# Kernel tuning notes

Hardware: AMD Instinct MI355X
Metric: run time of the kernel (lower is better)

Reference implementation:

```python
import jax, jax.numpy as jnp
import numpy as np

EMB_DIM = 512
HIDDEN = 512
NODE_DIM = 256
NUM_NODES = 64
L_RNN = 3
BATCH = 2048


def setup_inputs() -> dict:
    key = jax.random.key(0)
    ks = jax.random.split(key, 8)
    s = 0.05

    def rn(k, shape):
        return jax.random.normal(k, shape, dtype=jnp.float32) * s

    return {
        "emb": jax.random.normal(ks[0], (BATCH, EMB_DIM), dtype=jnp.float32),
        "Win1": rn(ks[1], (HIDDEN, EMB_DIM)),
        "bin1": jnp.zeros((HIDDEN,), jnp.float32),
        "Win2": rn(ks[2], (L_RNN * HIDDEN, HIDDEN)),
        "bin2": jnp.zeros((L_RNN * HIDDEN,), jnp.float32),
        "Wih": rn(ks[3], (L_RNN, 4 * HIDDEN, HIDDEN)),
        "Whh": rn(ks[4], (L_RNN, 4 * HIDDEN, HIDDEN)),
        "bih": jnp.zeros((L_RNN, 4 * HIDDEN), jnp.float32),
        "bhh": jnp.zeros((L_RNN, 4 * HIDDEN), jnp.float32),
        "Wout1": rn(ks[5], (HIDDEN, HIDDEN)),
        "bout1": jnp.zeros((HIDDEN,), jnp.float32),
        "Wout2": rn(ks[6], (NODE_DIM, HIDDEN)),
        "bout2": jnp.zeros((NODE_DIM,), jnp.float32),
    }


def reference(emb, Win1, bin1, Win2, bin2, Wih, Whh, bih, bhh,
              Wout1, bout1, Wout2, bout2):
    B = emb.shape[0]
    # FNN_in: emb -> initial hidden states for all LSTM layers
    hx = jax.nn.relu(emb @ Win1.T + bin1) @ Win2.T + bin2      # [B, L*H]
    hx = hx.reshape(B, L_RNN, HIDDEN).transpose(1, 0, 2)        # [L, B, H]
    cx = jnp.zeros_like(hx)
    x0 = jnp.zeros((B, HIDDEN), dtype=emb.dtype)                # first input (zeros)

    def step(carry, _):
        h, c, x = carry
        hs, cs = [], []
        inp = x
        for l in range(L_RNN):  # small fixed layer loop
            g = inp @ Wih[l].T + bih[l] + h[l] @ Whh[l].T + bhh[l]  # [B, 4H]
            i, f, gg, o = jnp.split(g, 4, axis=-1)  # PyTorch gate order i,f,g,o
            c_new = jax.nn.sigmoid(f) * c[l] + jax.nn.sigmoid(i) * jnp.tanh(gg)
            h_new = jax.nn.sigmoid(o) * jnp.tanh(c_new)
            hs.append(h_new)
            cs.append(c_new)
            inp = h_new
        return (jnp.stack(hs), jnp.stack(cs), inp), inp

    _, ys = jax.lax.scan(step, (hx, cx, x0), None, length=NUM_NODES)  # [T, B, H]

    x = ys.transpose(1, 0, 2).reshape(B * NUM_NODES, HIDDEN)    # [B*T, H]
    x = jax.nn.relu(x @ Wout1.T + bout1) @ Wout2.T + bout2      # FNN_out
    return x.reshape(B, NUM_NODES, NODE_DIM)
```

## Files before the change

### kernel.cpp

```cpp
#include <hip/hip_runtime.h>
#include <hip/hip_bf16.h>
#include <cstdint>
#include <cstddef>

using bf16 = __hip_bfloat16;
typedef short bf16x8 __attribute__((ext_vector_type(8)));
typedef float f32x4 __attribute__((ext_vector_type(4)));

#define CHUNK 16

__device__ __forceinline__ float fsigmoid(float x) {
  return 1.0f / (1.0f + __expf(-x));
}
__device__ __forceinline__ float ftanh_(float x) {
  float e = __expf(-2.0f * fabsf(x));
  float t = (1.0f - e) / (1.0f + e);
  return copysignf(t, x);
}

__device__ __forceinline__ void gload_lds16(const void* g, void* l) {
  __builtin_amdgcn_global_load_lds(
      (const __attribute__((address_space(1))) void*)g,
      (__attribute__((address_space(3))) void*)l, 16, 0, 0);
}

__global__ void cvt_bf16_kernel(const float* __restrict__ in, bf16* __restrict__ out, int n) {
  int i = blockIdx.x * blockDim.x + threadIdx.x;
  int stride = gridDim.x * blockDim.x;
  for (; i < n; i += stride) out[i] = __float2bfloat16(in[i]);
}

__global__ void build_wf_kernel(const float* __restrict__ Wih, const float* __restrict__ Whh,
                                const float* __restrict__ bih, const float* __restrict__ bhh,
                                bf16* __restrict__ Wf, float* __restrict__ bfused) {
  int i = blockIdx.x * 256 + threadIdx.x;
  int k = i & 1023;
  int r = (i >> 10) & 2047;
  int l = i >> 21;
  int u = r >> 6, gate = (r >> 4) & 3, v = r & 15;
  int j = u * 16 + v;
  int srow = l * 2048 + gate * 512 + j;
  float val = (k < 512) ? Wih[(size_t)srow * 512 + k] : Whh[(size_t)srow * 512 + (k - 512)];
  Wf[i] = __float2bfloat16(val);
  if (k == 0) bfused[l * 2048 + r] = bih[srow] + bhh[srow];
}

template <int EPI>
__global__ __launch_bounds__(512) void gemm_bt(
    const bf16* __restrict__ A0, const bf16* __restrict__ A1,
    const bf16* __restrict__ Bw, const float* __restrict__ bias,
    void* __restrict__ out0, void* __restrict__ out1, void* __restrict__ out2,
    float* __restrict__ cst,
    int K, int lda, int ldo, int aux) {
  const int tid = threadIdx.x;
  const int wave = tid >> 6;
  const int lane = tid & 63;

  const int gx = gridDim.x;
  const int nwg = gx * gridDim.y;
  const int flat = blockIdx.x + gx * blockIdx.y;
  int m0, n0;
  if (gx == 16 && gridDim.y == 16) {
    const int xcd = flat & 7;
    const int w = flat >> 3;
    const int mt = (xcd >> 2) * 8 + (w & 7);
    const int nt = (xcd & 3) * 4 + (w >> 3);
    m0 = mt * 128;
    n0 = nt * 128;
  } else {
    const int v = (flat & 7) * (nwg >> 3) + (flat >> 3);
    m0 = (v % gx) * 128;
    n0 = (v / gx) * 128;
  }

  const int wr = wave >> 1, wc = wave & 1;

  __shared__ alignas(16) short ls[4 * 16384];
  char* lsb = (char*)ls;

  f32x4 acc[2][4];
#pragma unroll
  for (int i = 0; i < 2; ++i)
#pragma unroll
    for (int j = 0; j < 4; ++j) acc[i][j] = (f32x4){0.f, 0.f, 0.f, 0.f};

  const int s_row = tid >> 3;
  const int s_k = (((tid & 7) ^ ((tid >> 3) & 7)) * 8);
  const int l16 = lane & 15;
  const int khi = lane >> 4;
  const int sx = l16 & 7;

  const int nk = K >> 6;

  auto stage = [&](int step) {
    int b = step & 3;
    int kt = step << 6;
    const bf16* as = A0;
    int kk = kt;
    if (kt >= 512) { as = A1; kk = kt - 512; }
    char* base = lsb + b * 32768;
    gload_lds16(as + (size_t)(m0 + s_row) * lda + kk + s_k, base + tid * 16);
    gload_lds16(as + (size_t)(m0 + 64 + s_row) * lda + kk + s_k, base + 8192 + tid * 16);
    gload_lds16(Bw + (size_t)(n0 + s_row) * K + kt + s_k, base + 16384 + tid * 16);
    gload_lds16(Bw + (size_t)(n0 + 64 + s_row) * K + kt + s_k, base + 24576 + tid * 16);
  };

  auto compute = [&](int step) {
    int b = step & 3;
    const short* LA = ls + b * 16384;
    const short* LB = LA + 8192;
    bf16x8 af[2][2], bv[4][2];
#pragma unroll
    for (int kk = 0; kk < 2; ++kk) {
      int pgA = ((kk * 4 + khi) ^ sx) * 8;
#pragma unroll
      for (int i = 0; i < 2; ++i)
        af[i][kk] = *(const bf16x8*)&LA[(wr * 32 + i * 16 + l16) * 64 + pgA];
#pragma unroll
      for (int i = 0; i < 4; ++i)
        bv[i][kk] = *(const bf16x8*)&LB[(wc * 64 + i * 16 + l16) * 64 + pgA];
    }
#pragma unroll
    for (int kk = 0; kk < 2; ++kk)
#pragma unroll
      for (int mi = 0; mi < 2; ++mi)
#pragma unroll
        for (int ni = 0; ni < 4; ++ni)
          acc[mi][ni] = __builtin_amdgcn_mfma_f32_16x16x32_bf16(af[mi][kk], bv[ni][kk], acc[mi][ni], 0, 0, 0);
  };

  stage(0);
  stage(1);
  for (int t = 0; t < nk - 2; ++t) {
    stage(t + 2);
    asm volatile("s_waitcnt vmcnt(8)" ::: "memory");
    __builtin_amdgcn_s_barrier();
    __builtin_amdgcn_sched_barrier(0);
    compute(t);
  }
  asm volatile("s_waitcnt vmcnt(4)" ::: "memory");
  __builtin_amdgcn_s_barrier();
  __builtin_amdgcn_sched_barrier(0);
  compute(nk - 2);
  asm volatile("s_waitcnt vmcnt(0)" ::: "memory");
  __builtin_amdgcn_s_barrier();
  __builtin_amdgcn_sched_barrier(0);
  compute(nk - 1);

  const int rbase = (lane >> 4) * 4;

  if constexpr (EPI == 0) {
    bf16* O = (bf16*)out0;
#pragma unroll
    for (int mi = 0; mi < 2; ++mi)
#pragma unroll
      for (int ni = 0; ni < 4; ++ni) {
        int col = n0 + wc * 64 + ni * 16 + l16;
        float bvv = bias[col];
#pragma unroll
        for (int r = 0; r < 4; ++r) {
          int row = m0 + wr * 32 + mi * 16 + rbase + r;
          float v2 = acc[mi][ni][r] + bvv;
          O[(size_t)row * ldo + col] = __float2bfloat16(fmaxf(v2, 0.f));
        }
      }
  } else if constexpr (EPI == 2) {
#pragma unroll
    for (int mi = 0; mi < 2; ++mi)
#pragma unroll
      for (int ni = 0; ni < 4; ++ni) {
        int col = n0 + wc * 64 + ni * 16 + l16;
        int lyr = col >> 9;
        bf16* O = (bf16*)(lyr == 0 ? out0 : (lyr == 1 ? out1 : out2));
        int j = col & 511;
        float bvv = bias[col];
#pragma unroll
        for (int r = 0; r < 4; ++r) {
          int row = m0 + wr * 32 + mi * 16 + rbase + r;
          O[(size_t)row * 512 + j] = __float2bfloat16(acc[mi][ni][r] + bvv);
        }
      }
  } else if constexpr (EPI == 3) {
    bf16* H = (bf16*)out0;
    bf16* Y = (bf16*)out1;
    int ucol = ((n0 >> 6) + wc) * 16 + l16;
    float bi = bias[n0 + wc * 64 + 0 + l16];
    float bff = bias[n0 + wc * 64 + 16 + l16];
    float bg = bias[n0 + wc * 64 + 32 + l16];
    float bo = bias[n0 + wc * 64 + 48 + l16];
#pragma unroll
    for (int mi = 0; mi < 2; ++mi)
#pragma unroll
      for (int r = 0; r < 4; ++r) {
        int row = m0 + wr * 32 + mi * 16 + rbase + r;
        float gi = acc[mi][0][r] + bi;
        float gf = acc[mi][1][r] + bff;
        float gg = acc[mi][2][r] + bg;
        float go = acc[mi][3][r] + bo;
        size_t idx = (size_t)row * 512 + ucol;
        float cold = cst[idx];
        float cn = fsigmoid(gf) * cold + fsigmoid(gi) * ftanh_(gg);
        float hn = fsigmoid(go) * ftanh_(cn);
        cst[idx] = cn;
        bf16 hb = __float2bfloat16(hn);
        H[idx] = hb;
        if (Y) Y[((size_t)row * CHUNK + aux) * 512 + ucol] = hb;
      }
  } else if constexpr (EPI == 4) {
    float* O = (float*)out0;
#pragma unroll
    for (int mi = 0; mi < 2; ++mi)
#pragma unroll
      for (int ni = 0; ni < 4; ++ni) {
        int col = n0 + wc * 64 + ni * 16 + l16;
        float bvv = bias[col];
#pragma unroll
        for (int r = 0; r < 4; ++r) {
          int row = m0 + wr * 32 + mi * 16 + rbase + r;
          int orow = ((row / CHUNK) << 6) + aux + (row % CHUNK);
          O[(size_t)orow * ldo + col] = acc[mi][ni][r] + bvv;
        }
      }
  }
}

extern "C" void kernel_launch(void* const* d_in, const int* in_sizes, int n_in,
                              void* d_out, int out_size, void* d_ws, size_t ws_size,
                              hipStream_t stream) {
  const float* emb = (const float*)d_in[0];
  const float* Win1 = (const float*)d_in[1];
  const float* bin1 = (const float*)d_in[2];
  const float* Win2 = (const float*)d_in[3];
  const float* bin2 = (const float*)d_in[4];
  const float* Wih = (const float*)d_in[5];
  const float* Whh = (const float*)d_in[6];
  const float* bih = (const float*)d_in[7];
  const float* bhh = (const float*)d_in[8];
  const float* Wout1 = (const float*)d_in[9];
  const float* bout1 = (const float*)d_in[10];
  const float* Wout2 = (const float*)d_in[11];
  const float* bout2 = (const float*)d_in[12];
  float* out = (float*)d_out;
  (void)in_sizes; (void)n_in; (void)out_size; (void)ws_size;

  char* p = (char*)d_ws;
  auto carve = [&](size_t bytes) {
    char* r = p;
    p += (bytes + 255) & ~(size_t)255;
    return r;
  };

  bf16* Wf = (bf16*)carve((size_t)3 * 2048 * 1024 * 2);
  float* bfuse = (float*)carve((size_t)3 * 2048 * 4);
  bf16* Win1b = (bf16*)carve((size_t)512 * 512 * 2);
  bf16* Win2b = (bf16*)carve((size_t)1536 * 512 * 2);
  bf16* Wout1b = (bf16*)carve((size_t)512 * 512 * 2);
  bf16* Wout2b = (bf16*)carve((size_t)256 * 512 * 2);
  bf16* embb = (bf16*)carve((size_t)2048 * 512 * 2);
  bf16* C1 = (bf16*)carve((size_t)2048 * 512 * 2);
  bf16* hbuf = (bf16*)carve((size_t)2 * 3 * 2048 * 512 * 2);
  float* cst = (float*)carve((size_t)3 * 2048 * 512 * 4);
  bf16* x0 = (bf16*)carve((size_t)2048 * 512 * 2);
  bf16* ysc = (bf16*)carve((size_t)2048 * CHUNK * 512 * 2);
  bf16* Z = (bf16*)carve((size_t)2048 * CHUNK * 512 * 2);

  hipMemsetAsync(cst, 0, (size_t)3 * 2048 * 512 * 4, stream);
  hipMemsetAsync(x0, 0, (size_t)2048 * 512 * 2, stream);

  cvt_bf16_kernel<<<1024, 256, 0, stream>>>(emb, embb, 2048 * 512);
  cvt_bf16_kernel<<<1024, 256, 0, stream>>>(Win1, Win1b, 512 * 512);
  cvt_bf16_kernel<<<1024, 256, 0, stream>>>(Win2, Win2b, 1536 * 512);
  cvt_bf16_kernel<<<1024, 256, 0, stream>>>(Wout1, Wout1b, 512 * 512);
  cvt_bf16_kernel<<<512, 256, 0, stream>>>(Wout2, Wout2b, 256 * 512);
  build_wf_kernel<<<(3 * 2048 * 1024) / 256, 256, 0, stream>>>(Wih, Whh, bih, bhh, Wf, bfuse);

  auto hset = [&](int s, int l) { return hbuf + ((size_t)s * 3 + l) * 2048 * 512; };

  gemm_bt<0><<<dim3(16, 4), 512, 0, stream>>>(embb, nullptr, Win1b, bin1,
                                              C1, nullptr, nullptr, nullptr, 512, 512, 512, 0);
  gemm_bt<2><<<dim3(16, 12), 512, 0, stream>>>(C1, nullptr, Win2b, bin2,
                                               hset(0, 0), hset(0, 1), hset(0, 2), nullptr,
                                               512, 512, 0, 0);

  for (int t = 0; t < 64; ++t) {
    int cur = t & 1;
    bf16* hR0 = hset(cur, 0);
    bf16* hR1 = hset(cur, 1);
    bf16* hR2 = hset(cur, 2);
    bf16* hW0 = hset(cur ^ 1, 0);
    bf16* hW1 = hset(cur ^ 1, 1);
    bf16* hW2 = hset(cur ^ 1, 2);
    const bf16* inp0 = (t == 0) ? (const bf16*)x0 : (const bf16*)hR2;
    int tc = t % CHUNK;

    gemm_bt<3><<<dim3(16, 16), 512, 0, stream>>>(inp0, hR0, Wf, bfuse,
                                                 hW0, nullptr, nullptr, cst,
                                                 1024, 512, 0, tc);
    gemm_bt<3><<<dim3(16, 16), 512, 0, stream>>>(hW0, hR1, Wf + (size_t)2048 * 1024, bfuse + 2048,
                                                 hW1, nullptr, nullptr, cst + (size_t)2048 * 512,
                                                 1024, 512, 0, tc);
    gemm_bt<3><<<dim3(16, 16), 512, 0, stream>>>(hW1, hR2, Wf + (size_t)2 * 2048 * 1024, bfuse + 2 * 2048,
                                                 hW2, ysc, nullptr, cst + (size_t)2 * 2048 * 512,
                                                 1024, 512, 0, tc);

    if (tc == CHUNK - 1) {
      gemm_bt<0><<<dim3(2048 * CHUNK / 128, 4), 512, 0, stream>>>(
          ysc, nullptr, Wout1b, bout1, Z, nullptr, nullptr, nullptr, 512, 512, 512, 0);
      gemm_bt<4><<<dim3(2048 * CHUNK / 128, 2), 512, 0, stream>>>(
          Z, nullptr, Wout2b, bout2, out, nullptr, nullptr, nullptr, 512, 512, 256, t - (CHUNK - 1));
    }
  }
}
```

Baseline: 3.004 ms.

## Load A fragments directly from global into registers instead of via LDS

The GEMM kernel now stages only the B tile through LDS with direct-to-LDS loads. Each wave reads its A fragments straight from global memory into registers, double-buffered across two k-steps. This halves LDS use and removes the A LDS reads, in exchange for uncoalesced per-lane 16-byte global loads and more register pressure. The loop is also restructured into pairs of steps with new vmcnt thresholds. The waits may be wrong, since the register-destined loads and the LDS loads share the same counter and a trailing step is conditional, which risks a race if nk is odd.

```diff
diff --git a/kernel.cpp b/kernel.cpp
--- a/kernel.cpp
+++ b/kernel.cpp
@@ -75,7 +75,7 @@
 
   const int wr = wave >> 1, wc = wave & 1;
 
-  __shared__ alignas(16) short ls[4 * 16384];
+  __shared__ alignas(16) short ls[4 * 8192];
   char* lsb = (char*)ls;
 
   f32x4 acc[2][4];
@@ -92,30 +92,39 @@
 
   const int nk = K >> 6;
 
-  auto stage = [&](int step) {
+  const size_t arow0 = (size_t)(m0 + wr * 32 + l16) * lda;
+  const size_t arow1 = (size_t)(m0 + wr * 32 + 16 + l16) * lda;
+  const int akoff = khi * 8;
+
+  auto stage_B = [&](int step) {
     int b = step & 3;
     int kt = step << 6;
+    char* base = lsb + b * 16384;
+    gload_lds16(Bw + (size_t)(n0 + s_row) * K + kt + s_k, base + tid * 16);
+    gload_lds16(Bw + (size_t)(n0 + 64 + s_row) * K + kt + s_k, base + 8192 + tid * 16);
+  };
+
+  struct AFrag { bf16x8 f[2][2]; };
+  auto load_A = [&](int step) {
+    AFrag r;
+    int kt = step << 6;
     const bf16* as = A0;
-    int kk = kt;
-    if (kt >= 512) { as = A1; kk = kt - 512; }
-    char* base = lsb + b * 32768;
-    gload_lds16(as + (size_t)(m0 + s_row) * lda + kk + s_k, base + tid * 16);
-    gload_lds16(as + (size_t)(m0 + 64 + s_row) * lda + kk + s_k, base + 8192 + tid * 16);
-    gload_lds16(Bw + (size_t)(n0 + s_row) * K + kt + s_k, base + 16384 + tid * 16);
-    gload_lds16(Bw + (size_t)(n0 + 64 + s_row) * K + kt + s_k, base + 24576 + tid * 16);
+    if (kt >= 512) { as = A1; kt -= 512; }
+#pragma unroll
+    for (int kk = 0; kk < 2; ++kk) {
+      r.f[0][kk] = *(const bf16x8*)(as + arow0 + kt + kk * 32 + akoff);
+      r.f[1][kk] = *(const bf16x8*)(as + arow1 + kt + kk * 32 + akoff);
+    }
+    return r;
   };
 
-  auto compute = [&](int step) {
+  auto compute = [&](int step, const AFrag& af) {
     int b = step & 3;
-    const short* LA = ls + b * 16384;
-    const short* LB = LA + 8192;
-    bf16x8 af[2][2], bv[4][2];
+    const short* LB = ls + b * 8192;
+    bf16x8 bv[4][2];
 #pragma unroll
     for (int kk = 0; kk < 2; ++kk) {
       int pgA = ((kk * 4 + khi) ^ sx) * 8;
-#pragma unroll
-      for (int i = 0; i < 2; ++i)
-        af[i][kk] = *(const bf16x8*)&LA[(wr * 32 + i * 16 + l16) * 64 + pgA];
 #pragma unroll
       for (int i = 0; i < 4; ++i)
         bv[i][kk] = *(const bf16x8*)&LB[(wc * 64 + i * 16 + l16) * 64 + pgA];
@@ -126,26 +135,39 @@
       for (int mi = 0; mi < 2; ++mi)
 #pragma unroll
         for (int ni = 0; ni < 4; ++ni)
-          acc[mi][ni] = __builtin_amdgcn_mfma_f32_16x16x32_bf16(af[mi][kk], bv[ni][kk], acc[mi][ni], 0, 0, 0);
+          acc[mi][ni] = __builtin_amdgcn_mfma_f32_16x16x32_bf16(af.f[mi][kk], bv[ni][kk], acc[mi][ni], 0, 0, 0);
   };
 
-  stage(0);
-  stage(1);
-  for (int t = 0; t < nk - 2; ++t) {
-    stage(t + 2);
-    asm volatile("s_waitcnt vmcnt(8)" ::: "memory");
+  stage_B(0);
+  AFrag pA = load_A(0);
+  stage_B(1);
+  AFrag pB = load_A(1);
+
+  for (int t = 0; t < nk - 2; t += 2) {
+    asm volatile("s_waitcnt vmcnt(6)" ::: "memory");
     __builtin_amdgcn_s_barrier();
     __builtin_amdgcn_sched_barrier(0);
-    compute(t);
+    compute(t, pA);
+    stage_B(t + 2);
+    pA = load_A(t + 2);
+
+    asm volatile("s_waitcnt vmcnt(6)" ::: "memory");
+    __builtin_amdgcn_s_barrier();
+    __builtin_amdgcn_sched_barrier(0);
+    compute(t + 1, pB);
+    if (t + 3 < nk) {
+      stage_B(t + 3);
+      pB = load_A(t + 3);
+    }
   }
-  asm volatile("s_waitcnt vmcnt(4)" ::: "memory");
+  asm volatile("s_waitcnt vmcnt(6)" ::: "memory");
   __builtin_amdgcn_s_barrier();
   __builtin_amdgcn_sched_barrier(0);
-  compute(nk - 2);
+  compute(nk - 2, pA);
   asm volatile("s_waitcnt vmcnt(0)" ::: "memory");
   __builtin_amdgcn_s_barrier();
   __builtin_amdgcn_sched_barrier(0);
-  compute(nk - 1);
+  compute(nk - 1, pB);
 
   const int rbase = (lane >> 4) * 4;
 
```

Measured after the change: 4.479 ms. 1.49x slower.

## Interleave half-tile global-to-LDS loads with MFMA halves and raise CHUNK

Applied to the files above, without the earlier changes.

Splits each k-step's LDS staging and MFMA compute into two halves, issuing the next stage's A and B loads between compute halves instead of before the wait. MFMA sections run under raised wave priority via s_setprio. The wait count drops from 8 to 4 outstanding loads, and CHUNK goes from 16 to 64, which likely changes how many timesteps each batched GEMM launch covers. The aim is better overlap of memory and matrix work and fewer launches, at the cost of tighter scheduling assumptions and possible LDS buffer hazards if the waits are wrong.

```diff
diff --git a/kernel.cpp b/kernel.cpp
--- a/kernel.cpp
+++ b/kernel.cpp
@@ -7,7 +7,7 @@
 typedef short bf16x8 __attribute__((ext_vector_type(8)));
 typedef float f32x4 __attribute__((ext_vector_type(4)));
 
-#define CHUNK 16
+#define CHUNK 64
 
 __device__ __forceinline__ float fsigmoid(float x) {
   return 1.0f / (1.0f + __expf(-x));
@@ -92,60 +92,64 @@
 
   const int nk = K >> 6;
 
-  auto stage = [&](int step) {
+  auto stage_half = [&](int step, int half) {
     int b = step & 3;
     int kt = step << 6;
-    const bf16* as = A0;
-    int kk = kt;
-    if (kt >= 512) { as = A1; kk = kt - 512; }
     char* base = lsb + b * 32768;
-    gload_lds16(as + (size_t)(m0 + s_row) * lda + kk + s_k, base + tid * 16);
-    gload_lds16(as + (size_t)(m0 + 64 + s_row) * lda + kk + s_k, base + 8192 + tid * 16);
-    gload_lds16(Bw + (size_t)(n0 + s_row) * K + kt + s_k, base + 16384 + tid * 16);
-    gload_lds16(Bw + (size_t)(n0 + 64 + s_row) * K + kt + s_k, base + 24576 + tid * 16);
+    if (half == 0) {
+      const bf16* as = A0;
+      int kk = kt;
+      if (kt >= 512) { as = A1; kk = kt - 512; }
+      gload_lds16(as + (size_t)(m0 + s_row) * lda + kk + s_k, base + tid * 16);
+      gload_lds16(as + (size_t)(m0 + 64 + s_row) * lda + kk + s_k, base + 8192 + tid * 16);
+    } else {
+      gload_lds16(Bw + (size_t)(n0 + s_row) * K + kt + s_k, base + 16384 + tid * 16);
+      gload_lds16(Bw + (size_t)(n0 + 64 + s_row) * K + kt + s_k, base + 24576 + tid * 16);
+    }
   };
 
-  auto compute = [&](int step) {
+  auto compute_half = [&](int step, int kk) {
     int b = step & 3;
     const short* LA = ls + b * 16384;
     const short* LB = LA + 8192;
-    bf16x8 af[2][2], bv[4][2];
-#pragma unroll
-    for (int kk = 0; kk < 2; ++kk) {
-      int pgA = ((kk * 4 + khi) ^ sx) * 8;
-#pragma unroll
-      for (int i = 0; i < 2; ++i)
-        af[i][kk] = *(const bf16x8*)&LA[(wr * 32 + i * 16 + l16) * 64 + pgA];
-#pragma unroll
-      for (int i = 0; i < 4; ++i)
-        bv[i][kk] = *(const bf16x8*)&LB[(wc * 64 + i * 16 + l16) * 64 + pgA];
-    }
-#pragma unroll
-    for (int kk = 0; kk < 2; ++kk)
-#pragma unroll
-      for (int mi = 0; mi < 2; ++mi)
-#pragma unroll
-        for (int ni = 0; ni < 4; ++ni)
-          acc[mi][ni] = __builtin_amdgcn_mfma_f32_16x16x32_bf16(af[mi][kk], bv[ni][kk], acc[mi][ni], 0, 0, 0);
+    bf16x8 af[2], bv[4];
+    int pgA = ((kk * 4 + khi) ^ sx) * 8;
+#pragma unroll
+    for (int i = 0; i < 2; ++i)
+      af[i] = *(const bf16x8*)&LA[(wr * 32 + i * 16 + l16) * 64 + pgA];
+#pragma unroll
+    for (int i = 0; i < 4; ++i)
+      bv[i] = *(const bf16x8*)&LB[(wc * 64 + i * 16 + l16) * 64 + pgA];
+    __builtin_amdgcn_s_setprio(1);
+#pragma unroll
+    for (int mi = 0; mi < 2; ++mi)
+#pragma unroll
+      for (int ni = 0; ni < 4; ++ni)
+        acc[mi][ni] = __builtin_amdgcn_mfma_f32_16x16x32_bf16(af[mi], bv[ni], acc[mi][ni], 0, 0, 0);
+    __builtin_amdgcn_s_setprio(0);
   };
 
-  stage(0);
-  stage(1);
+  stage_half(0, 0); stage_half(0, 1);
+  stage_half(1, 0); stage_half(1, 1);
   for (int t = 0; t < nk - 2; ++t) {
-    stage(t + 2);
-    asm volatile("s_waitcnt vmcnt(8)" ::: "memory");
+    asm volatile("s_waitcnt vmcnt(4)" ::: "memory");
     __builtin_amdgcn_s_barrier();
     __builtin_amdgcn_sched_barrier(0);
-    compute(t);
+    compute_half(t, 0);
+    stage_half(t + 2, 0);
+    compute_half(t, 1);
+    stage_half(t + 2, 1);
   }
   asm volatile("s_waitcnt vmcnt(4)" ::: "memory");
   __builtin_amdgcn_s_barrier();
   __builtin_amdgcn_sched_barrier(0);
-  compute(nk - 2);
+  compute_half(nk - 2, 0);
+  compute_half(nk - 2, 1);
   asm volatile("s_waitcnt vmcnt(0)" ::: "memory");
   __builtin_amdgcn_s_barrier();
   __builtin_amdgcn_sched_barrier(0);
-  compute(nk - 1);
+  compute_half(nk - 1, 0);
+  compute_half(nk - 1, 1);
 
   const int rbase = (lane >> 4) * 4;
 
```

After: 2.995 ms. No clear change (-0.3%).
